# Kernel optimization log

Measured on AMD Instinct MI355X. Metric: run time of the kernel, lower is better.

The kernel has to match this reference:

```python
import jax, jax.numpy as jnp
import numpy as np


def gcn_layer(x, src, dst, deg_inv_sqrt, W, b):
    # PyG GCNConv: h = X W; out[i] = sum_{j->i} norm(j,i) * h[j] + deg_i^{-1} * h[i] + b
    n = x.shape[0]
    h = x @ W                                   # [N, out]
    norm = deg_inv_sqrt[src] * deg_inv_sqrt[dst]  # [E]
    msg = h[src] * norm[:, None]                # [E, out]
    agg = jax.ops.segment_sum(msg, dst, num_segments=n)
    # self-loop contribution (added loops with norm = deg_i^{-1})
    agg = agg + h * (deg_inv_sqrt * deg_inv_sqrt)[:, None]
    return agg + b


def setup_inputs() -> dict:
    key = jax.random.key(0)
    k1, k2, k3, k4, k5, k6 = jax.random.split(key, 6)
    N, E, IN, HID, OUT = 50000, 800000, 128, 128, 64
    x = jax.random.normal(k1, (N, IN), dtype=jnp.float32)
    edge_index = jax.random.randint(k2, (2, E), 0, N, dtype=jnp.int64)
    # glorot-ish init for weights, zeros-ish bias
    W1 = jax.random.normal(k3, (IN, HID), dtype=jnp.float32) * (1.0 / np.sqrt(IN))
    b1 = jax.random.normal(k4, (HID,), dtype=jnp.float32) * 0.01
    W2 = jax.random.normal(k5, (HID, OUT), dtype=jnp.float32) * (1.0 / np.sqrt(HID))
    b2 = jax.random.normal(k6, (OUT,), dtype=jnp.float32) * 0.01
    return {"x": x, "edge_index": edge_index, "W1": W1, "b1": b1, "W2": W2, "b2": b2}


def reference(x, edge_index, W1, b1, W2, b2):
    n = x.shape[0]
    src, dst = edge_index[0], edge_index[1]
    # degree with self-loops (PyG computes degree on the dst/col index)
    deg = jax.ops.segment_sum(jnp.ones_like(dst, dtype=x.dtype), dst, num_segments=n) + 1.0
    deg_inv_sqrt = jax.lax.rsqrt(deg)
    h = gcn_layer(x, src, dst, deg_inv_sqrt, W1, b1)
    h = jax.nn.relu(h)
    # F.dropout with training=False is identity (module evaluated in eval mode)
    out = gcn_layer(h, src, dst, deg_inv_sqrt, W2, b2)
    return out
```

## Files before the change

kernel.cpp:

```cpp
#include <hip/hip_runtime.h>
#include <stdint.h>

typedef __attribute__((ext_vector_type(8))) short short8;
typedef __attribute__((ext_vector_type(4))) float floatx4;

static inline size_t align256(size_t x) { return (x + 255) & ~size_t(255); }

__device__ __forceinline__ unsigned short f2bf(float f) {
    unsigned u = __float_as_uint(f);
    u += 0x7fff + ((u >> 16) & 1);
    return (unsigned short)(u >> 16);
}
__device__ __forceinline__ unsigned pack_bf16(float a, float b) {
    return (unsigned)f2bf(a) | ((unsigned)f2bf(b) << 16);
}
__device__ __forceinline__ float bf_lo(unsigned u) { return __uint_as_float(u << 16); }
__device__ __forceinline__ float bf_hi(unsigned u) { return __uint_as_float(u & 0xffff0000u); }

#define BSHIFT 7
#define NBMAX 1024
#define CH 2048
#define SCAP 3072

__device__ __forceinline__ bool detect_i32(const void* eidx, int E, int t) {
    const long long* e64 = (const long long*)eidx;
    int nchk = E < 256 ? E : 256;
    long long v = e64[t % nchk];
    int bad = (v < 0 || v > 0x7fffffffLL) ? 1 : 0;
    return __syncthreads_or(bad) != 0;
}

__global__ __launch_bounds__(256) void k_hist(const void* __restrict__ eidx, int E,
        int* __restrict__ chist, int NB, int NC,
        const float* __restrict__ W1, const float* __restrict__ W2,
        unsigned short* __restrict__ w1t, unsigned short* __restrict__ w2t,
        int K1, int M1, int K2, int M2) {
    __shared__ int hist[NBMAX];
    const int t = threadIdx.x, B = blockIdx.x;
    if (B < NC) {
        const int e0 = B * CH;
        const int e1 = (e0 + CH < E) ? e0 + CH : E;
        const bool i32 = detect_i32(eidx, E, t);
        const int* e32 = (const int*)eidx;
        const long long* e64 = (const long long*)eidx;
        for (int b0 = 0; b0 < NB; b0 += NBMAX) {
            int bw = (NB - b0 < NBMAX) ? NB - b0 : NBMAX;
            for (int i = t; i < bw; i += 256) hist[i] = 0;
            __syncthreads();
            for (int e = e0 + t; e < e1; e += 256) {
                int d = i32 ? e32[(size_t)E + e] : (int)e64[(size_t)E + e];
                int b = (d >> BSHIFT) - b0;
                if (b >= 0 && b < bw) atomicAdd(&hist[b], 1);
            }
            __syncthreads();
            for (int i = t; i < bw; i += 256) chist[(size_t)(b0 + i) * NC + B] = hist[i];
            __syncthreads();
        }
    } else if (B == NC) {
        for (int j = t; j < K1 * M1; j += 256) {
            int k = j / M1, n = j % M1;
            w1t[(size_t)n * K1 + k] = f2bf(W1[j]);
        }
    } else if (B == NC + 1) {
        for (int j = t; j < K2 * M2; j += 256) {
            int k = j / M2, n = j % M2;
            w2t[(size_t)n * K2 + k] = f2bf(W2[j]);
        }
    }
}

__global__ __launch_bounds__(256) void k_btot(const int* __restrict__ chist,
                                              int* __restrict__ btot, int NB, int NC) {
    int b = blockIdx.x * 4 + (threadIdx.x >> 6);
    if (b >= NB) return;
    int lane = threadIdx.x & 63;
    const int* row = chist + (size_t)b * NC;
    int v = 0;
    for (int i = lane; i < NC; i += 64) v += row[i];
    #pragma unroll
    for (int off = 32; off >= 1; off >>= 1) v += __shfl_xor(v, off, 64);
    if (lane == 0) btot[b] = v;
}

__global__ __launch_bounds__(1024) void k_bscan(const int* __restrict__ btot,
                                                int* __restrict__ bbase,
                                                int* __restrict__ rs_final,
                                                int NB, int N) {
    __shared__ int swt[16];
    const int t = threadIdx.x, lane = t & 63, w = t >> 6;
    int carry = 0;
    for (int base = 0; base < NB; base += 1024) {
        int i = base + t;
        int v = (i < NB) ? btot[i] : 0;
        int incl = v;
        #pragma unroll
        for (int off = 1; off < 64; off <<= 1) {
            int nbr = __shfl_up(incl, off, 64);
            if (lane >= off) incl += nbr;
        }
        if (lane == 63) swt[w] = incl;
        __syncthreads();
        int woff = 0;
        for (int j = 0; j < w; ++j) woff += swt[j];
        if (i < NB) bbase[i] = carry + woff + incl - v;
        int tot = 0;
        for (int j = 0; j < 16; ++j) tot += swt[j];
        carry += tot;
        __syncthreads();
    }
    if (t == 0) { bbase[NB] = carry; rs_final[N] = carry; }
}

__global__ __launch_bounds__(256) void k_hscan2(int* __restrict__ chist,
                                                const int* __restrict__ bbase,
                                                int NB, int NC) {
    int b = blockIdx.x * 4 + (threadIdx.x >> 6);
    if (b >= NB) return;
    int lane = threadIdx.x & 63;
    int* row = chist + (size_t)b * NC;
    int carry = bbase[b];
    for (int base = 0; base < NC; base += 64) {
        int i = base + lane;
        int v = (i < NC) ? row[i] : 0;
        int incl = v;
        #pragma unroll
        for (int off = 1; off < 64; off <<= 1) {
            int nbr = __shfl_up(incl, off, 64);
            if (lane >= off) incl += nbr;
        }
        if (i < NC) row[i] = carry + incl - v;
        carry += __shfl(incl, 63, 64);
    }
}

__global__ __launch_bounds__(256) void k_bfill(const void* __restrict__ eidx, int E,
                                               const int* __restrict__ chist,
                                               unsigned* __restrict__ bbuf, int NB, int NC) {
    __shared__ int rank[NBMAX];
    __shared__ int base[NBMAX];
    const int t = threadIdx.x, c = blockIdx.x;
    const int e0 = c * CH;
    const int e1 = (e0 + CH < E) ? e0 + CH : E;
    const bool i32 = detect_i32(eidx, E, t);
    const int* e32 = (const int*)eidx;
    const long long* e64 = (const long long*)eidx;
    for (int b0 = 0; b0 < NB; b0 += NBMAX) {
        int bw = (NB - b0 < NBMAX) ? NB - b0 : NBMAX;
        for (int i = t; i < bw; i += 256) {
            rank[i] = 0;
            base[i] = chist[(size_t)(b0 + i) * NC + c];
        }
        __syncthreads();
        for (int e = e0 + t; e < e1; e += 256) {
            int s, d;
            if (i32) { s = e32[e]; d = e32[(size_t)E + e]; }
            else     { s = (int)e64[e]; d = (int)e64[(size_t)E + e]; }
            int b = (d >> BSHIFT) - b0;
            if (b >= 0 && b < bw) {
                int slot = base[b] + atomicAdd(&rank[b], 1);
                bbuf[slot] = ((unsigned)(d & 127) << 25) | (unsigned)s;
            }
        }
        __syncthreads();
    }
}

__global__ __launch_bounds__(256) void k_sort(const unsigned* __restrict__ bbuf,
                                              const int* __restrict__ bbase,
                                              int* __restrict__ rs_final,
                                              float* __restrict__ dinv,
                                              int* __restrict__ esrc, int N) {
    __shared__ int hist[128];
    __shared__ int off[128];
    __shared__ int srcbuf[SCAP];
    const int b = blockIdx.x, t = threadIdx.x;
    const int node0 = b << BSHIFT;
    const int nloc = (N - node0 < 128) ? N - node0 : 128;
    const int s0 = bbase[b], s1 = bbase[b + 1];
    const int cnt = s1 - s0;
    if (t < 128) hist[t] = 0;
    __syncthreads();
    for (int i = s0 + t; i < s1; i += 256)
        atomicAdd(&hist[bbuf[i] >> 25], 1);
    __syncthreads();
    if (t < 64) {
        int carry = 0;
        #pragma unroll
        for (int base = 0; base < 128; base += 64) {
            int v = hist[base + t];
            int incl = v;
            #pragma unroll
            for (int o = 1; o < 64; o <<= 1) {
                int nbr = __shfl_up(incl, o, 64);
                if (t >= o) incl += nbr;
            }
            off[base + t] = carry + incl - v;
            carry += __shfl(incl, 63, 64);
        }
    }
    __syncthreads();
    if (t < nloc) {
        rs_final[node0 + t] = s0 + off[t];
        dinv[node0 + t] = rsqrtf((float)hist[t] + 1.0f);
    }
    __syncthreads();
    if (t < 128) hist[t] = 0;
    __syncthreads();
    if (cnt <= SCAP) {
        for (int i = s0 + t; i < s1; i += 256) {
            unsigned sd = bbuf[i];
            int lo = sd >> 25;
            int r = atomicAdd(&hist[lo], 1);
            srcbuf[off[lo] + r] = (int)(sd & 0x1ffffffu);
        }
        __syncthreads();
        for (int i = t; i < cnt; i += 256) esrc[s0 + i] = srcbuf[i];
    } else {
        for (int i = s0 + t; i < s1; i += 256) {
            unsigned sd = bbuf[i];
            int lo = sd >> 25;
            int r = atomicAdd(&hist[lo], 1);
            esrc[s0 + off[lo] + r] = (int)(sd & 0x1ffffffu);
        }
    }
}

template<int BN, bool AF32>
__global__ __launch_bounds__(256, 3) void k_gemm(
        const void* __restrict__ Av, const unsigned short* __restrict__ Bt,
        const float* __restrict__ dinv, unsigned short* __restrict__ C,
        int N, int M) {
    constexpr int LD = 136;
    __shared__ unsigned short As[64 * LD];
    __shared__ unsigned short Bs[BN * LD];
    const int tid = threadIdx.x;
    const int wave = tid >> 6, lane = tid & 63;
    const int q = lane >> 4, tm = lane & 15;
    const int row0 = blockIdx.x * 64;

    {
        const uint4* Bg = (const uint4*)Bt;
        #pragma unroll
        for (int it = 0; it < BN / 16; ++it) {
            int i = tid + it * 256;
            int r = i >> 4, o = i & 15;
            *(uint4*)&Bs[r * LD + o * 8] = Bg[(size_t)r * 16 + o];
        }
    }
    if (AF32) {
        const float4* Ag = (const float4*)Av;
        #pragma unroll
        for (int it = 0; it < 8; ++it) {
            int i = tid + it * 256;
            int r = i >> 5, o = i & 31;
            int row = row0 + r;
            float4 v = make_float4(0.f, 0.f, 0.f, 0.f);
            if (row < N) v = Ag[(size_t)row * 32 + o];
            uint2 pk;
            pk.x = pack_bf16(v.x, v.y);
            pk.y = pack_bf16(v.z, v.w);
            *(uint2*)&As[r * LD + o * 4] = pk;
        }
    } else {
        const uint4* Ag = (const uint4*)Av;
        #pragma unroll
        for (int it = 0; it < 4; ++it) {
            int i = tid + it * 256;
            int r = i >> 4, o = i & 15;
            int row = row0 + r;
            uint4 v = make_uint4(0, 0, 0, 0);
            if (row < N) v = Ag[(size_t)row * 16 + o];
            *(uint4*)&As[r * LD + o * 8] = v;
        }
    }
    __syncthreads();

    constexpr int NG = BN / 16;
    floatx4 acc[NG];
    #pragma unroll
    for (int g = 0; g < NG; ++g) acc[g] = (floatx4){0.f, 0.f, 0.f, 0.f};

    const int arow = wave * 16 + tm;
    #pragma unroll
    for (int kc = 0; kc < 4; ++kc) {
        short8 af = *(const short8*)&As[arow * LD + kc * 32 + q * 8];
        #pragma unroll
        for (int g = 0; g < NG; ++g) {
            short8 bf = *(const short8*)&Bs[(g * 16 + tm) * LD + kc * 32 + q * 8];
            acc[g] = __builtin_amdgcn_mfma_f32_16x16x32_bf16(af, bf, acc[g], 0, 0, 0);
        }
    }

    float dv[4];
    #pragma unroll
    for (int r = 0; r < 4; ++r) {
        int row = row0 + wave * 16 + q * 4 + r;
        dv[r] = (row < N) ? dinv[row] : 0.f;
    }
    #pragma unroll
    for (int g = 0; g < NG; ++g) {
        #pragma unroll
        for (int r = 0; r < 4; ++r) {
            int row = row0 + wave * 16 + q * 4 + r;
            if (row < N) C[(size_t)row * M + g * 16 + tm] = f2bf(dv[r] * acc[g][r]);
        }
    }
}

__global__ __launch_bounds__(256) void k_agg128(const unsigned* __restrict__ Hb,
        const float* __restrict__ dinv, const int* __restrict__ rs,
        const int* __restrict__ esrc, const float* __restrict__ bias,
        uint2* __restrict__ out, int N) {
    int wid = (blockIdx.x * 256 + threadIdx.x) >> 6;
    if (wid >= N) return;
    int l = threadIdx.x & 63;
    int hi = l >> 5;
    int q  = l & 31;
    const uint2* H2 = (const uint2*)Hb;
    float di = dinv[wid];
    float a0 = 0.f, a1 = 0.f, a2 = 0.f, a3 = 0.f;
    int k = rs[wid], kend = rs[wid + 1];
    for (; k + 8 <= kend; k += 8) {
        int s[4];
        #pragma unroll
        for (int j = 0; j < 4; ++j) s[j] = esrc[k + 2 * j + hi];
        uint2 g[4];
        #pragma unroll
        for (int j = 0; j < 4; ++j) g[j] = H2[(size_t)s[j] * 32 + q];
        #pragma unroll
        for (int j = 0; j < 4; ++j) {
            a0 += bf_lo(g[j].x); a1 += bf_hi(g[j].x);
            a2 += bf_lo(g[j].y); a3 += bf_hi(g[j].y);
        }
    }
    if (k + 4 <= kend) {
        int s[2];
        #pragma unroll
        for (int j = 0; j < 2; ++j) s[j] = esrc[k + 2 * j + hi];
        uint2 g[2];
        #pragma unroll
        for (int j = 0; j < 2; ++j) g[j] = H2[(size_t)s[j] * 32 + q];
        #pragma unroll
        for (int j = 0; j < 2; ++j) {
            a0 += bf_lo(g[j].x); a1 += bf_hi(g[j].x);
            a2 += bf_lo(g[j].y); a3 += bf_hi(g[j].y);
        }
        k += 4;
    }
    if (k + 2 <= kend) {
        int s = esrc[k + hi];
        uint2 g = H2[(size_t)s * 32 + q];
        a0 += bf_lo(g.x); a1 += bf_hi(g.x);
        a2 += bf_lo(g.y); a3 += bf_hi(g.y);
        k += 2;
    }
    if (k < kend && hi == 0) {
        int s = esrc[k];
        uint2 g = H2[(size_t)s * 32 + q];
        a0 += bf_lo(g.x); a1 += bf_hi(g.x);
        a2 += bf_lo(g.y); a3 += bf_hi(g.y);
    }
    a0 += __shfl_xor(a0, 32, 64);
    a1 += __shfl_xor(a1, 32, 64);
    a2 += __shfl_xor(a2, 32, 64);
    a3 += __shfl_xor(a3, 32, 64);
    uint2 sr = H2[(size_t)wid * 32 + q];
    a0 += bf_lo(sr.x); a1 += bf_hi(sr.x);
    a2 += bf_lo(sr.y); a3 += bf_hi(sr.y);
    float4 b = ((const float4*)bias)[q];
    float o0 = fmaxf(fmaf(di, a0, b.x), 0.f);
    float o1 = fmaxf(fmaf(di, a1, b.y), 0.f);
    float o2 = fmaxf(fmaf(di, a2, b.z), 0.f);
    float o3 = fmaxf(fmaf(di, a3, b.w), 0.f);
    if (hi == 0) {
        uint2 pk;
        pk.x = pack_bf16(o0, o1);
        pk.y = pack_bf16(o2, o3);
        out[(size_t)wid * 32 + q] = pk;
    }
}

__global__ __launch_bounds__(256) void k_agg64(const unsigned short* __restrict__ Hb,
        const float* __restrict__ dinv, const int* __restrict__ rs,
        const int* __restrict__ esrc, const float* __restrict__ bias,
        float2* __restrict__ out, int N) {
    int wid = (blockIdx.x * 256 + threadIdx.x) >> 6;
    if (wid >= N) return;
    int l = threadIdx.x & 63;
    int hi = l >> 5;
    int q  = l & 31;
    const unsigned* H1 = (const unsigned*)Hb;
    float di = dinv[wid];
    float a0 = 0.f, a1 = 0.f;
    int k = rs[wid], kend = rs[wid + 1];
    for (; k + 8 <= kend; k += 8) {
        int s[4];
        #pragma unroll
        for (int j = 0; j < 4; ++j) s[j] = esrc[k + 2 * j + hi];
        unsigned g[4];
        #pragma unroll
        for (int j = 0; j < 4; ++j) g[j] = H1[(size_t)s[j] * 32 + q];
        #pragma unroll
        for (int j = 0; j < 4; ++j) { a0 += bf_lo(g[j]); a1 += bf_hi(g[j]); }
    }
    if (k + 4 <= kend) {
        int s[2];
        #pragma unroll
        for (int j = 0; j < 2; ++j) s[j] = esrc[k + 2 * j + hi];
        unsigned g[2];
        #pragma unroll
        for (int j = 0; j < 2; ++j) g[j] = H1[(size_t)s[j] * 32 + q];
        #pragma unroll
        for (int j = 0; j < 2; ++j) { a0 += bf_lo(g[j]); a1 += bf_hi(g[j]); }
        k += 4;
    }
    if (k + 2 <= kend) {
        int s = esrc[k + hi];
        unsigned g = H1[(size_t)s * 32 + q];
        a0 += bf_lo(g); a1 += bf_hi(g);
        k += 2;
    }
    if (k < kend && hi == 0) {
        unsigned g = H1[(size_t)esrc[k] * 32 + q];
        a0 += bf_lo(g); a1 += bf_hi(g);
    }
    a0 += __shfl_xor(a0, 32, 64);
    a1 += __shfl_xor(a1, 32, 64);
    unsigned sr = H1[(size_t)wid * 32 + q];
    a0 += bf_lo(sr); a1 += bf_hi(sr);
    float2 b = ((const float2*)bias)[q];
    if (hi == 0) {
        float2 o;
        o.x = fmaf(di, a0, b.x);
        o.y = fmaf(di, a1, b.y);
        out[(size_t)wid * 32 + q] = o;
    }
}

extern "C" void kernel_launch(void* const* d_in, const int* in_sizes, int n_in,
                              void* d_out, int out_size, void* d_ws, size_t ws_size,
                              hipStream_t stream) {
    const float* x  = (const float*)d_in[0];
    const void*  ei = d_in[1];
    const float* W1 = (const float*)d_in[2];
    const float* b1 = (const float*)d_in[3];
    const float* W2 = (const float*)d_in[4];
    const float* b2 = (const float*)d_in[5];

    int HID = in_sizes[3];
    int IN  = in_sizes[2] / HID;
    int OUT = in_sizes[4] / HID;
    int N   = in_sizes[0] / IN;
    int E   = in_sizes[1] / 2;
    int NB  = (N + 127) >> BSHIFT;
    int NC  = (E + CH - 1) / CH;

    char* p = (char*)d_ws;
    int* chist     = (int*)p;   p += align256((size_t)NB * NC * 4);
    int* btot      = (int*)p;   p += align256((size_t)NB * 4);
    int* bbase     = (int*)p;   p += align256((size_t)(NB + 1) * 4);
    int* rs_final  = (int*)p;   p += align256((size_t)(N + 1) * 4);
    int* esrc      = (int*)p;   p += align256((size_t)E * 4);
    float* dinv    = (float*)p; p += align256((size_t)N * 4);
    unsigned short* w1t = (unsigned short*)p; p += align256((size_t)HID * IN * 2);
    unsigned short* w2t = (unsigned short*)p; p += align256((size_t)OUT * HID * 2);
    size_t hb_bytes = (size_t)N * HID * 2, bbuf_bytes = (size_t)E * 4;
    unsigned* bbuf = (unsigned*)p;
    unsigned short* hb = (unsigned short*)p;
    p += align256(hb_bytes > bbuf_bytes ? hb_bytes : bbuf_bytes);
    unsigned short* h1b = (unsigned short*)p; p += align256((size_t)N * HID * 2);
    unsigned short* h2b = (unsigned short*)p; p += align256((size_t)N * OUT * 2);

    k_hist<<<NC + 2, 256, 0, stream>>>(ei, E, chist, NB, NC,
                                       W1, W2, w1t, w2t, IN, HID, HID, OUT);
    k_btot<<<(NB + 3) / 4, 256, 0, stream>>>(chist, btot, NB, NC);
    k_bscan<<<1, 1024, 0, stream>>>(btot, bbase, rs_final, NB, N);
    k_hscan2<<<(NB + 3) / 4, 256, 0, stream>>>(chist, bbase, NB, NC);
    k_bfill<<<NC, 256, 0, stream>>>(ei, E, chist, bbuf, NB, NC);
    k_sort<<<NB, 256, 0, stream>>>(bbuf, bbase, rs_final, dinv, esrc, N);

    k_gemm<128, true><<<(N + 63) / 64, 256, 0, stream>>>(x, w1t, dinv, hb, N, HID);
    k_agg128<<<(N + 3) / 4, 256, 0, stream>>>((unsigned*)hb, dinv, rs_final, esrc, b1,
                                              (uint2*)h1b, N);

    k_gemm<64, false><<<(N + 63) / 64, 256, 0, stream>>>(h1b, w2t, dinv, h2b, N, OUT);
    k_agg64<<<(N + 3) / 4, 256, 0, stream>>>(h2b, dinv, rs_final, esrc, b2,
                                             (float2*)d_out, N);
}
```

Measured before the change: 209.9 us.

## Replace bucketed two-level CSR sort with atomic degree count, decoupled-lookback scan, atomic fill

The CSR build is rewritten. Previously it used a bucketed counting sort: a per-chunk histogram, a bucket scan, a histogram scan, a bucket fill and a per-bucket local sort. Now it uses global atomic degree counting, a single-pass decoupled-lookback prefix scan, and an atomic-cursor scatter of source indices. This cuts the launch count from six to four and removes the large NB×NC histogram traffic. The cost is heavy global atomic contention and non-deterministic edge order within each row, which can change the floating-point summation order in the aggregation kernels.

```diff
diff --git a/kernel.cpp b/kernel.cpp
--- a/kernel.cpp
+++ b/kernel.cpp
@@ -17,10 +17,7 @@
 __device__ __forceinline__ float bf_lo(unsigned u) { return __uint_as_float(u << 16); }
 __device__ __forceinline__ float bf_hi(unsigned u) { return __uint_as_float(u & 0xffff0000u); }
 
-#define BSHIFT 7
-#define NBMAX 1024
 #define CH 2048
-#define SCAP 3072
 
 __device__ __forceinline__ bool detect_i32(const void* eidx, int E, int t) {
     const long long* e64 = (const long long*)eidx;
@@ -30,198 +27,125 @@
     return __syncthreads_or(bad) != 0;
 }
 
-__global__ __launch_bounds__(256) void k_hist(const void* __restrict__ eidx, int E,
-        int* __restrict__ chist, int NB, int NC,
+__global__ __launch_bounds__(256) void k_init(int* __restrict__ cnt, int N,
+        int* __restrict__ tb, long long* __restrict__ partials, int NT,
         const float* __restrict__ W1, const float* __restrict__ W2,
         unsigned short* __restrict__ w1t, unsigned short* __restrict__ w2t,
         int K1, int M1, int K2, int M2) {
-    __shared__ int hist[NBMAX];
+    int gid = blockIdx.x * 256 + threadIdx.x;
+    int tot = gridDim.x * 256;
+    for (int i = gid; i < N; i += tot) cnt[i] = 0;
+    if (gid == 0) *tb = 0;
+    for (int i = gid; i < NT; i += tot) partials[i] = 0;
+    for (int j = gid; j < K1 * M1; j += tot) {
+        int k = j / M1, n = j % M1;
+        w1t[(size_t)n * K1 + k] = f2bf(W1[j]);
+    }
+    for (int j = gid; j < K2 * M2; j += tot) {
+        int k = j / M2, n = j % M2;
+        w2t[(size_t)n * K2 + k] = f2bf(W2[j]);
+    }
+}
+
+__global__ __launch_bounds__(256) void k_deg(const void* __restrict__ eidx, int E,
+                                             int* __restrict__ cnt) {
     const int t = threadIdx.x, B = blockIdx.x;
-    if (B < NC) {
-        const int e0 = B * CH;
-        const int e1 = (e0 + CH < E) ? e0 + CH : E;
-        const bool i32 = detect_i32(eidx, E, t);
-        const int* e32 = (const int*)eidx;
-        const long long* e64 = (const long long*)eidx;
-        for (int b0 = 0; b0 < NB; b0 += NBMAX) {
-            int bw = (NB - b0 < NBMAX) ? NB - b0 : NBMAX;
-            for (int i = t; i < bw; i += 256) hist[i] = 0;
-            __syncthreads();
-            for (int e = e0 + t; e < e1; e += 256) {
-                int d = i32 ? e32[(size_t)E + e] : (int)e64[(size_t)E + e];
-                int b = (d >> BSHIFT) - b0;
-                if (b >= 0 && b < bw) atomicAdd(&hist[b], 1);
-            }
-            __syncthreads();
-            for (int i = t; i < bw; i += 256) chist[(size_t)(b0 + i) * NC + B] = hist[i];
-            __syncthreads();
-        }
-    } else if (B == NC) {
-        for (int j = t; j < K1 * M1; j += 256) {
-            int k = j / M1, n = j % M1;
-            w1t[(size_t)n * K1 + k] = f2bf(W1[j]);
-        }
-    } else if (B == NC + 1) {
-        for (int j = t; j < K2 * M2; j += 256) {
-            int k = j / M2, n = j % M2;
-            w2t[(size_t)n * K2 + k] = f2bf(W2[j]);
-        }
-    }
-}
-
-__global__ __launch_bounds__(256) void k_btot(const int* __restrict__ chist,
-                                              int* __restrict__ btot, int NB, int NC) {
-    int b = blockIdx.x * 4 + (threadIdx.x >> 6);
-    if (b >= NB) return;
-    int lane = threadIdx.x & 63;
-    const int* row = chist + (size_t)b * NC;
-    int v = 0;
-    for (int i = lane; i < NC; i += 64) v += row[i];
-    #pragma unroll
-    for (int off = 32; off >= 1; off >>= 1) v += __shfl_xor(v, off, 64);
-    if (lane == 0) btot[b] = v;
-}
-
-__global__ __launch_bounds__(1024) void k_bscan(const int* __restrict__ btot,
-                                                int* __restrict__ bbase,
-                                                int* __restrict__ rs_final,
-                                                int NB, int N) {
-    __shared__ int swt[16];
-    const int t = threadIdx.x, lane = t & 63, w = t >> 6;
-    int carry = 0;
-    for (int base = 0; base < NB; base += 1024) {
-        int i = base + t;
-        int v = (i < NB) ? btot[i] : 0;
-        int incl = v;
-        #pragma unroll
-        for (int off = 1; off < 64; off <<= 1) {
-            int nbr = __shfl_up(incl, off, 64);
-            if (lane >= off) incl += nbr;
-        }
-        if (lane == 63) swt[w] = incl;
-        __syncthreads();
-        int woff = 0;
-        for (int j = 0; j < w; ++j) woff += swt[j];
-        if (i < NB) bbase[i] = carry + woff + incl - v;
-        int tot = 0;
-        for (int j = 0; j < 16; ++j) tot += swt[j];
-        carry += tot;
-        __syncthreads();
-    }
-    if (t == 0) { bbase[NB] = carry; rs_final[N] = carry; }
-}
-
-__global__ __launch_bounds__(256) void k_hscan2(int* __restrict__ chist,
-                                                const int* __restrict__ bbase,
-                                                int NB, int NC) {
-    int b = blockIdx.x * 4 + (threadIdx.x >> 6);
-    if (b >= NB) return;
-    int lane = threadIdx.x & 63;
-    int* row = chist + (size_t)b * NC;
-    int carry = bbase[b];
-    for (int base = 0; base < NC; base += 64) {
-        int i = base + lane;
-        int v = (i < NC) ? row[i] : 0;
-        int incl = v;
-        #pragma unroll
-        for (int off = 1; off < 64; off <<= 1) {
-            int nbr = __shfl_up(incl, off, 64);
-            if (lane >= off) incl += nbr;
-        }
-        if (i < NC) row[i] = carry + incl - v;
-        carry += __shfl(incl, 63, 64);
-    }
-}
-
-__global__ __launch_bounds__(256) void k_bfill(const void* __restrict__ eidx, int E,
-                                               const int* __restrict__ chist,
-                                               unsigned* __restrict__ bbuf, int NB, int NC) {
-    __shared__ int rank[NBMAX];
-    __shared__ int base[NBMAX];
-    const int t = threadIdx.x, c = blockIdx.x;
-    const int e0 = c * CH;
+    const int e0 = B * CH;
     const int e1 = (e0 + CH < E) ? e0 + CH : E;
     const bool i32 = detect_i32(eidx, E, t);
     const int* e32 = (const int*)eidx;
     const long long* e64 = (const long long*)eidx;
-    for (int b0 = 0; b0 < NB; b0 += NBMAX) {
-        int bw = (NB - b0 < NBMAX) ? NB - b0 : NBMAX;
-        for (int i = t; i < bw; i += 256) {
-            rank[i] = 0;
-            base[i] = chist[(size_t)(b0 + i) * NC + c];
-        }
-        __syncthreads();
-        for (int e = e0 + t; e < e1; e += 256) {
-            int s, d;
-            if (i32) { s = e32[e]; d = e32[(size_t)E + e]; }
-            else     { s = (int)e64[e]; d = (int)e64[(size_t)E + e]; }
-            int b = (d >> BSHIFT) - b0;
-            if (b >= 0 && b < bw) {
-                int slot = base[b] + atomicAdd(&rank[b], 1);
-                bbuf[slot] = ((unsigned)(d & 127) << 25) | (unsigned)s;
+    for (int e = e0 + t; e < e1; e += 256) {
+        int d = i32 ? e32[(size_t)E + e] : (int)e64[(size_t)E + e];
+        atomicAdd(&cnt[d], 1);
+    }
+}
+
+__device__ __forceinline__ long long pack_sv(int status, int value) {
+    return ((long long)status << 32) | (unsigned)value;
+}
+__global__ __launch_bounds__(256) void k_scan(const int* __restrict__ cnt,
+        int* __restrict__ rs, int* __restrict__ cursor, float* __restrict__ dinv,
+        int N, int E, int* __restrict__ tb, long long* __restrict__ partials, int NT) {
+    __shared__ int s_tile;
+    __shared__ int wsum[4];
+    __shared__ int s_excl;
+    const int t = threadIdx.x, lane = t & 63, w = t >> 6;
+    if (t == 0) s_tile = atomicAdd(tb, 1);
+    __syncthreads();
+    const int tile = s_tile;
+    const int idx = tile * 1024 + t * 4;
+    int v0 = 0, v1 = 0, v2 = 0, v3 = 0;
+    if (idx + 4 <= N) {
+        int4 q = *(const int4*)&cnt[idx];
+        v0 = q.x; v1 = q.y; v2 = q.z; v3 = q.w;
+    } else {
+        if (idx + 0 < N) v0 = cnt[idx + 0];
+        if (idx + 1 < N) v1 = cnt[idx + 1];
+        if (idx + 2 < N) v2 = cnt[idx + 2];
+        if (idx + 3 < N) v3 = cnt[idx + 3];
+    }
+    int tsum = v0 + v1 + v2 + v3;
+    int incl = tsum;
+    #pragma unroll
+    for (int off = 1; off < 64; off <<= 1) {
+        int nbr = __shfl_up(incl, off, 64);
+        if (lane >= off) incl += nbr;
+    }
+    if (lane == 63) wsum[w] = incl;
+    __syncthreads();
+    int woff = 0;
+    for (int j = 0; j < w; ++j) woff += wsum[j];
+    int agg = wsum[0] + wsum[1] + wsum[2] + wsum[3];
+    int texcl = woff + incl - tsum;
+    if (t == 0) {
+        if (tile == 0) {
+            __hip_atomic_store(&partials[0], pack_sv(2, agg),
+                               __ATOMIC_RELEASE, __HIP_MEMORY_SCOPE_AGENT);
+            s_excl = 0;
+            rs[N] = E;
+        } else {
+            __hip_atomic_store(&partials[tile], pack_sv(1, agg),
+                               __ATOMIC_RELEASE, __HIP_MEMORY_SCOPE_AGENT);
+            int excl = 0;
+            for (int p = tile - 1; p >= 0; ) {
+                long long pv;
+                do {
+                    pv = __hip_atomic_load(&partials[p],
+                                           __ATOMIC_ACQUIRE, __HIP_MEMORY_SCOPE_AGENT);
+                } while ((int)(pv >> 32) == 0);
+                excl += (int)(unsigned)(pv & 0xffffffffLL);
+                if ((int)(pv >> 32) == 2) break;
+                --p;
             }
-        }
-        __syncthreads();
-    }
-}
-
-__global__ __launch_bounds__(256) void k_sort(const unsigned* __restrict__ bbuf,
-                                              const int* __restrict__ bbase,
-                                              int* __restrict__ rs_final,
-                                              float* __restrict__ dinv,
-                                              int* __restrict__ esrc, int N) {
-    __shared__ int hist[128];
-    __shared__ int off[128];
-    __shared__ int srcbuf[SCAP];
-    const int b = blockIdx.x, t = threadIdx.x;
-    const int node0 = b << BSHIFT;
-    const int nloc = (N - node0 < 128) ? N - node0 : 128;
-    const int s0 = bbase[b], s1 = bbase[b + 1];
-    const int cnt = s1 - s0;
-    if (t < 128) hist[t] = 0;
+            __hip_atomic_store(&partials[tile], pack_sv(2, excl + agg),
+                               __ATOMIC_RELEASE, __HIP_MEMORY_SCOPE_AGENT);
+            s_excl = excl;
+        }
+    }
     __syncthreads();
-    for (int i = s0 + t; i < s1; i += 256)
-        atomicAdd(&hist[bbuf[i] >> 25], 1);
-    __syncthreads();
-    if (t < 64) {
-        int carry = 0;
-        #pragma unroll
-        for (int base = 0; base < 128; base += 64) {
-            int v = hist[base + t];
-            int incl = v;
-            #pragma unroll
-            for (int o = 1; o < 64; o <<= 1) {
-                int nbr = __shfl_up(incl, o, 64);
-                if (t >= o) incl += nbr;
-            }
-            off[base + t] = carry + incl - v;
-            carry += __shfl(incl, 63, 64);
-        }
-    }
-    __syncthreads();
-    if (t < nloc) {
-        rs_final[node0 + t] = s0 + off[t];
-        dinv[node0 + t] = rsqrtf((float)hist[t] + 1.0f);
-    }
-    __syncthreads();
-    if (t < 128) hist[t] = 0;
-    __syncthreads();
-    if (cnt <= SCAP) {
-        for (int i = s0 + t; i < s1; i += 256) {
-            unsigned sd = bbuf[i];
-            int lo = sd >> 25;
-            int r = atomicAdd(&hist[lo], 1);
-            srcbuf[off[lo] + r] = (int)(sd & 0x1ffffffu);
-        }
-        __syncthreads();
-        for (int i = t; i < cnt; i += 256) esrc[s0 + i] = srcbuf[i];
-    } else {
-        for (int i = s0 + t; i < s1; i += 256) {
-            unsigned sd = bbuf[i];
-            int lo = sd >> 25;
-            int r = atomicAdd(&hist[lo], 1);
-            esrc[s0 + off[lo] + r] = (int)(sd & 0x1ffffffu);
-        }
+    int ex = s_excl + texcl;
+    if (idx + 0 < N) { rs[idx + 0] = ex; cursor[idx + 0] = ex; dinv[idx + 0] = rsqrtf((float)v0 + 1.0f); ex += v0; }
+    if (idx + 1 < N) { rs[idx + 1] = ex; cursor[idx + 1] = ex; dinv[idx + 1] = rsqrtf((float)v1 + 1.0f); ex += v1; }
+    if (idx + 2 < N) { rs[idx + 2] = ex; cursor[idx + 2] = ex; dinv[idx + 2] = rsqrtf((float)v2 + 1.0f); ex += v2; }
+    if (idx + 3 < N) { rs[idx + 3] = ex; cursor[idx + 3] = ex; dinv[idx + 3] = rsqrtf((float)v3 + 1.0f); }
+}
+
+__global__ __launch_bounds__(256) void k_fill(const void* __restrict__ eidx, int E,
+                                              int* __restrict__ cursor,
+                                              int* __restrict__ esrc) {
+    const int t = threadIdx.x, B = blockIdx.x;
+    const int e0 = B * CH;
+    const int e1 = (e0 + CH < E) ? e0 + CH : E;
+    const bool i32 = detect_i32(eidx, E, t);
+    const int* e32 = (const int*)eidx;
+    const long long* e64 = (const long long*)eidx;
+    for (int e = e0 + t; e < e1; e += 256) {
+        int s, d;
+        if (i32) { s = e32[e]; d = e32[(size_t)E + e]; }
+        else     { s = (int)e64[e]; d = (int)e64[(size_t)E + e]; }
+        int slot = atomicAdd(&cursor[d], 1);
+        esrc[slot] = s;
     }
 }
 
@@ -452,32 +376,28 @@
     int OUT = in_sizes[4] / HID;
     int N   = in_sizes[0] / IN;
     int E   = in_sizes[1] / 2;
-    int NB  = (N + 127) >> BSHIFT;
     int NC  = (E + CH - 1) / CH;
+    int NT  = (N + 1023) >> 10;
 
     char* p = (char*)d_ws;
-    int* chist     = (int*)p;   p += align256((size_t)NB * NC * 4);
-    int* btot      = (int*)p;   p += align256((size_t)NB * 4);
-    int* bbase     = (int*)p;   p += align256((size_t)(NB + 1) * 4);
+    int* cnt       = (int*)p;   p += align256((size_t)N * 4);
     int* rs_final  = (int*)p;   p += align256((size_t)(N + 1) * 4);
+    int* cursor    = (int*)p;   p += align256((size_t)N * 4);
+    float* dinv    = (float*)p; p += align256((size_t)N * 4);
     int* esrc      = (int*)p;   p += align256((size_t)E * 4);
-    float* dinv    = (float*)p; p += align256((size_t)N * 4);
+    int* tb        = (int*)p;   p += align256(256);
+    long long* partials = (long long*)p; p += align256((size_t)NT * 8);
     unsigned short* w1t = (unsigned short*)p; p += align256((size_t)HID * IN * 2);
     unsigned short* w2t = (unsigned short*)p; p += align256((size_t)OUT * HID * 2);
-    size_t hb_bytes = (size_t)N * HID * 2, bbuf_bytes = (size_t)E * 4;
-    unsigned* bbuf = (unsigned*)p;
-    unsigned short* hb = (unsigned short*)p;
-    p += align256(hb_bytes > bbuf_bytes ? hb_bytes : bbuf_bytes);
+    unsigned short* hb  = (unsigned short*)p; p += align256((size_t)N * HID * 2);
     unsigned short* h1b = (unsigned short*)p; p += align256((size_t)N * HID * 2);
     unsigned short* h2b = (unsigned short*)p; p += align256((size_t)N * OUT * 2);
 
-    k_hist<<<NC + 2, 256, 0, stream>>>(ei, E, chist, NB, NC,
-                                       W1, W2, w1t, w2t, IN, HID, HID, OUT);
-    k_btot<<<(NB + 3) / 4, 256, 0, stream>>>(chist, btot, NB, NC);
-    k_bscan<<<1, 1024, 0, stream>>>(btot, bbase, rs_final, NB, N);
-    k_hscan2<<<(NB + 3) / 4, 256, 0, stream>>>(chist, bbase, NB, NC);
-    k_bfill<<<NC, 256, 0, stream>>>(ei, E, chist, bbuf, NB, NC);
-    k_sort<<<NB, 256, 0, stream>>>(bbuf, bbase, rs_final, dinv, esrc, N);
+    k_init<<<96, 256, 0, stream>>>(cnt, N, tb, partials, NT,
+                                   W1, W2, w1t, w2t, IN, HID, HID, OUT);
+    k_deg<<<NC, 256, 0, stream>>>(ei, E, cnt);
+    k_scan<<<NT, 256, 0, stream>>>(cnt, rs_final, cursor, dinv, N, E, tb, partials, NT);
+    k_fill<<<NC, 256, 0, stream>>>(ei, E, cursor, esrc);
 
     k_gemm<128, true><<<(N + 63) / 64, 256, 0, stream>>>(x, w1t, dinv, hb, N, HID);
     k_agg128<<<(N + 3) / 4, 256, 0, stream>>>((unsigned*)hb, dinv, rs_final, esrc, b1,
```

Result: slower. 255.6 us (+21.8%).

## Fuse CSR build stages into one cooperative kernel with grid syncs

Applied to the files above, without the earlier changes.

Replaces six separate launches (histogram, bucket totals, bucket scan, per-chunk scan, bucket fill, in-bucket sort) with a single cooperative kernel that separates the phases with grid.sync(). It is meant to remove launch gaps and per-kernel ramp-up across the preprocessing chain. Grid size is max(NB, NC), about 391 blocks here, so all blocks must be co-resident, and some phases leave many blocks idle. If the cooperative launch fails, the old multi-kernel path runs instead.

```diff
diff --git a/kernel.cpp b/kernel.cpp
--- a/kernel.cpp
+++ b/kernel.cpp
@@ -1,5 +1,8 @@
 #include <hip/hip_runtime.h>
+#include <hip/hip_cooperative_groups.h>
 #include <stdint.h>
+
+namespace cg = cooperative_groups;
 
 typedef __attribute__((ext_vector_type(8))) short short8;
 typedef __attribute__((ext_vector_type(4))) float floatx4;
@@ -21,6 +24,7 @@
 #define NBMAX 1024
 #define CH 2048
 #define SCAP 3072
+#define SHW 3328
 
 __device__ __forceinline__ bool detect_i32(const void* eidx, int E, int t) {
     const long long* e64 = (const long long*)eidx;
@@ -28,6 +32,192 @@
     long long v = e64[t % nchk];
     int bad = (v < 0 || v > 0x7fffffffLL) ? 1 : 0;
     return __syncthreads_or(bad) != 0;
+}
+
+__device__ __forceinline__ int blockScanExcl(int v, int t, int* sw, int* tot) {
+    int lane = t & 63, w = t >> 6;
+    int incl = v;
+    #pragma unroll
+    for (int off = 1; off < 64; off <<= 1) {
+        int nbr = __shfl_up(incl, off, 64);
+        if (lane >= off) incl += nbr;
+    }
+    if (lane == 63) sw[w] = incl;
+    __syncthreads();
+    int woff = 0;
+    for (int j = 0; j < w; ++j) woff += sw[j];
+    int tt = sw[0] + sw[1] + sw[2] + sw[3];
+    __syncthreads();
+    *tot = tt;
+    return woff + incl - v;
+}
+
+__global__ __launch_bounds__(256, 2) void k_csr(
+        const void* __restrict__ eidx, int E, int N, int NB, int NC,
+        int* __restrict__ chist, int* __restrict__ btot, int* __restrict__ bbase,
+        int* __restrict__ rs, float* __restrict__ dinv,
+        unsigned* __restrict__ bbuf, int* __restrict__ esrc,
+        const float* __restrict__ W1, const float* __restrict__ W2,
+        unsigned short* __restrict__ w1t, unsigned short* __restrict__ w2t,
+        int K1, int M1, int K2, int M2) {
+    cg::grid_group grid = cg::this_grid();
+    __shared__ int sh[SHW];
+    __shared__ int sw[4];
+    const int t = threadIdx.x, B = blockIdx.x;
+    const int gid = B * 256 + t, gtot = gridDim.x * 256;
+    const bool i32 = detect_i32(eidx, E, t);
+    const int* e32 = (const int*)eidx;
+    const long long* e64 = (const long long*)eidx;
+
+    if (B < NC) {
+        const int e0 = B * CH;
+        const int e1 = (e0 + CH < E) ? e0 + CH : E;
+        for (int b0 = 0; b0 < NB; b0 += SHW) {
+            int bw = (NB - b0 < SHW) ? NB - b0 : SHW;
+            for (int i = t; i < bw; i += 256) sh[i] = 0;
+            __syncthreads();
+            for (int e = e0 + t; e < e1; e += 256) {
+                int d = i32 ? e32[(size_t)E + e] : (int)e64[(size_t)E + e];
+                int b = (d >> BSHIFT) - b0;
+                if (b >= 0 && b < bw) atomicAdd(&sh[b], 1);
+            }
+            __syncthreads();
+            for (int i = t; i < bw; i += 256) chist[(size_t)(b0 + i) * NC + B] = sh[i];
+            __syncthreads();
+        }
+    }
+    for (int j = gid; j < K1 * M1; j += gtot) {
+        int k = j / M1, n = j % M1;
+        w1t[(size_t)n * K1 + k] = f2bf(W1[j]);
+    }
+    for (int j = gid; j < K2 * M2; j += gtot) {
+        int k = j / M2, n = j % M2;
+        w2t[(size_t)n * K2 + k] = f2bf(W2[j]);
+    }
+    grid.sync();
+
+    if (B < NB) {
+        const int* row = chist + (size_t)B * NC;
+        int v = 0;
+        for (int i = t; i < NC; i += 256) v += row[i];
+        int lane = t & 63, w = t >> 6;
+        #pragma unroll
+        for (int off = 32; off >= 1; off >>= 1) v += __shfl_xor(v, off, 64);
+        if (lane == 0) sw[w] = v;
+        __syncthreads();
+        if (t == 0) btot[B] = sw[0] + sw[1] + sw[2] + sw[3];
+    }
+    grid.sync();
+
+    if (B == 0) {
+        int carry = 0;
+        for (int base = 0; base < NB; base += 256) {
+            int i = base + t;
+            int v = (i < NB) ? btot[i] : 0;
+            int tot;
+            int ex = blockScanExcl(v, t, sw, &tot);
+            if (i < NB) bbase[i] = carry + ex;
+            carry += tot;
+        }
+        if (t == 0) { bbase[NB] = carry; rs[N] = carry; }
+    }
+    grid.sync();
+
+    if (B < NB) {
+        int* row = chist + (size_t)B * NC;
+        int carry = bbase[B];
+        for (int base = 0; base < NC; base += 256) {
+            int i = base + t;
+            int v = (i < NC) ? row[i] : 0;
+            int tot;
+            int ex = blockScanExcl(v, t, sw, &tot);
+            if (i < NC) row[i] = carry + ex;
+            carry += tot;
+        }
+    }
+    grid.sync();
+
+    if (B < NC) {
+        const int e0 = B * CH;
+        const int e1 = (e0 + CH < E) ? e0 + CH : E;
+        int* rank = sh;
+        int* base = sh + SHW / 2;
+        for (int b0 = 0; b0 < NB; b0 += SHW / 2) {
+            int bw = (NB - b0 < SHW / 2) ? NB - b0 : SHW / 2;
+            for (int i = t; i < bw; i += 256) {
+                rank[i] = 0;
+                base[i] = chist[(size_t)(b0 + i) * NC + B];
+            }
+            __syncthreads();
+            for (int e = e0 + t; e < e1; e += 256) {
+                int s, d;
+                if (i32) { s = e32[e]; d = e32[(size_t)E + e]; }
+                else     { s = (int)e64[e]; d = (int)e64[(size_t)E + e]; }
+                int b = (d >> BSHIFT) - b0;
+                if (b >= 0 && b < bw) {
+                    int slot = base[b] + atomicAdd(&rank[b], 1);
+                    bbuf[slot] = ((unsigned)(d & 127) << 25) | (unsigned)s;
+                }
+            }
+            __syncthreads();
+        }
+    }
+    grid.sync();
+
+    if (B < NB) {
+        int* hist = sh;
+        int* off  = sh + 128;
+        int* srcbuf = sh + 256;
+        const int node0 = B << BSHIFT;
+        const int nloc = (N - node0 < 128) ? N - node0 : 128;
+        const int s0 = bbase[B], s1 = bbase[B + 1];
+        const int cnt = s1 - s0;
+        if (t < 128) hist[t] = 0;
+        __syncthreads();
+        for (int i = s0 + t; i < s1; i += 256)
+            atomicAdd(&hist[bbuf[i] >> 25], 1);
+        __syncthreads();
+        if (t < 64) {
+            int carry = 0;
+            #pragma unroll
+            for (int base2 = 0; base2 < 128; base2 += 64) {
+                int v = hist[base2 + t];
+                int incl = v;
+                #pragma unroll
+                for (int o = 1; o < 64; o <<= 1) {
+                    int nbr = __shfl_up(incl, o, 64);
+                    if (t >= o) incl += nbr;
+                }
+                off[base2 + t] = carry + incl - v;
+                carry += __shfl(incl, 63, 64);
+            }
+        }
+        __syncthreads();
+        if (t < nloc) {
+            rs[node0 + t] = s0 + off[t];
+            dinv[node0 + t] = rsqrtf((float)hist[t] + 1.0f);
+        }
+        __syncthreads();
+        if (t < 128) hist[t] = 0;
+        __syncthreads();
+        if (cnt <= SCAP) {
+            for (int i = s0 + t; i < s1; i += 256) {
+                unsigned sd = bbuf[i];
+                int lo = sd >> 25;
+                int r = atomicAdd(&hist[lo], 1);
+                srcbuf[off[lo] + r] = (int)(sd & 0x1ffffffu);
+            }
+            __syncthreads();
+            for (int i = t; i < cnt; i += 256) esrc[s0 + i] = srcbuf[i];
+        } else {
+            for (int i = s0 + t; i < s1; i += 256) {
+                unsigned sd = bbuf[i];
+                int lo = sd >> 25;
+                int r = atomicAdd(&hist[lo], 1);
+                esrc[s0 + off[lo] + r] = (int)(sd & 0x1ffffffu);
+            }
+        }
+    }
 }
 
 __global__ __launch_bounds__(256) void k_hist(const void* __restrict__ eidx, int E,
@@ -440,8 +630,8 @@
 extern "C" void kernel_launch(void* const* d_in, const int* in_sizes, int n_in,
                               void* d_out, int out_size, void* d_ws, size_t ws_size,
                               hipStream_t stream) {
+    const void*  ei = d_in[1];
     const float* x  = (const float*)d_in[0];
-    const void*  ei = d_in[1];
     const float* W1 = (const float*)d_in[2];
     const float* b1 = (const float*)d_in[3];
     const float* W2 = (const float*)d_in[4];
@@ -471,13 +661,24 @@
     unsigned short* h1b = (unsigned short*)p; p += align256((size_t)N * HID * 2);
     unsigned short* h2b = (unsigned short*)p; p += align256((size_t)N * OUT * 2);
 
-    k_hist<<<NC + 2, 256, 0, stream>>>(ei, E, chist, NB, NC,
-                                       W1, W2, w1t, w2t, IN, HID, HID, OUT);
-    k_btot<<<(NB + 3) / 4, 256, 0, stream>>>(chist, btot, NB, NC);
-    k_bscan<<<1, 1024, 0, stream>>>(btot, bbase, rs_final, NB, N);
-    k_hscan2<<<(NB + 3) / 4, 256, 0, stream>>>(chist, bbase, NB, NC);
-    k_bfill<<<NC, 256, 0, stream>>>(ei, E, chist, bbuf, NB, NC);
-    k_sort<<<NB, 256, 0, stream>>>(bbuf, bbase, rs_final, dinv, esrc, N);
+    int G = NB > NC ? NB : NC;
+    int K1v = IN, M1v = HID, K2v = HID, M2v = OUT;
+    void* args[] = { (void*)&ei, &E, &N, &NB, &NC,
+                     (void*)&chist, (void*)&btot, (void*)&bbase,
+                     (void*)&rs_final, (void*)&dinv, (void*)&bbuf, (void*)&esrc,
+                     (void*)&W1, (void*)&W2, (void*)&w1t, (void*)&w2t,
+                     &K1v, &M1v, &K2v, &M2v };
+    hipError_t cerr = hipLaunchCooperativeKernel((const void*)k_csr,
+                                                 dim3(G), dim3(256), args, 0, stream);
+    if (cerr != hipSuccess) {
+        k_hist<<<NC + 2, 256, 0, stream>>>(ei, E, chist, NB, NC,
+                                           W1, W2, w1t, w2t, IN, HID, HID, OUT);
+        k_btot<<<(NB + 3) / 4, 256, 0, stream>>>(chist, btot, NB, NC);
+        k_bscan<<<1, 1024, 0, stream>>>(btot, bbase, rs_final, NB, N);
+        k_hscan2<<<(NB + 3) / 4, 256, 0, stream>>>(chist, bbase, NB, NC);
+        k_bfill<<<NC, 256, 0, stream>>>(ei, E, chist, bbuf, NB, NC);
+        k_sort<<<NB, 256, 0, stream>>>(bbuf, bbase, rs_final, dinv, esrc, N);
+    }
 
     k_gemm<128, true><<<(N + 63) / 64, 256, 0, stream>>>(x, w1t, dinv, hb, N, HID);
     k_agg128<<<(N + 3) / 4, 256, 0, stream>>>((unsigned*)hb, dinv, rs_final, esrc, b1,
```

New measurement: 447.5 us. 2.13x slower.
